# Kernel optimization log

Hardware: AMD Instinct MI355X
Metric: run time of the kernel (lower is better)

## Reference

```python
import jax, jax.numpy as jnp
import numpy as np

N_NODES = 100000
N_EDGES = 1600000
IN_F = 16
C1, C2 = 32, 64
HID = 128
N_CLASSES = 10
NUM_LAYERS = 3


def setup_inputs() -> dict:
    key = jax.random.key(0)
    ks = jax.random.split(key, 20)
    s = 0.1
    inp = {
        "x": jax.random.normal(ks[0], (N_NODES, IN_F), dtype=jnp.float32),
        "edge_index": jax.random.randint(ks[1], (2, N_EDGES), 0, N_NODES, dtype=jnp.int64),
        "edge_attr": jax.random.uniform(ks[2], (N_EDGES, 1), dtype=jnp.float32),
        # conv1 (out=32): per-step weight [L, 32, 32], GRUCell params
        "W1": jax.random.normal(ks[3], (NUM_LAYERS, C1, C1), dtype=jnp.float32) * s,
        "Wih1": jax.random.normal(ks[4], (3 * C1, C1), dtype=jnp.float32) * s,
        "Whh1": jax.random.normal(ks[5], (3 * C1, C1), dtype=jnp.float32) * s,
        "bih1": jnp.zeros((3 * C1,), dtype=jnp.float32),
        "bhh1": jnp.zeros((3 * C1,), dtype=jnp.float32),
        # conv2 (out=64)
        "W2": jax.random.normal(ks[6], (NUM_LAYERS, C2, C2), dtype=jnp.float32) * s,
        "Wih2": jax.random.normal(ks[7], (3 * C2, C2), dtype=jnp.float32) * s,
        "Whh2": jax.random.normal(ks[8], (3 * C2, C2), dtype=jnp.float32) * s,
        "bih2": jnp.zeros((3 * C2,), dtype=jnp.float32),
        "bhh2": jnp.zeros((3 * C2,), dtype=jnp.float32),
        # MLP head
        "fc1_w": jax.random.normal(ks[9], (HID, C2), dtype=jnp.float32) * s,
        "fc1_b": jnp.zeros((HID,), dtype=jnp.float32),
        "fc2_w": jax.random.normal(ks[10], (N_CLASSES, HID), dtype=jnp.float32) * s,
        "fc2_b": jnp.zeros((N_CLASSES,), dtype=jnp.float32),
    }
    return inp


def _gru_cell(m, h, Wih, Whh, bih, bhh):
    gi = m @ Wih.T + bih
    gh = h @ Whh.T + bhh
    ir, iz, inn = jnp.split(gi, 3, axis=1)
    hr, hz, hn = jnp.split(gh, 3, axis=1)
    r = jax.nn.sigmoid(ir + hr)
    z = jax.nn.sigmoid(iz + hz)
    n = jnp.tanh(inn + r * hn)
    return (1.0 - z) * n + z * h


def _gated_graph_conv(x, edge_index, edge_weight, W, Wih, Whh, bih, bhh):
    # PyG GatedGraphConv with aggr='max'
    n, c = x.shape
    out_ch = W.shape[-1]
    h = jnp.pad(x, ((0, 0), (0, out_ch - c))) if c < out_ch else x
    src, dst = edge_index[0], edge_index[1]
    ew = edge_weight[:, None]
    for i in range(W.shape[0]):
        m = h @ W[i]
        msg = m[src] * ew                      # [E, out_ch] gather + scale
        agg = jax.ops.segment_max(msg, dst, num_segments=n)  # scatter-max
        agg = jnp.where(jnp.isfinite(agg), agg, 0.0)         # empty segs -> 0
        h = _gru_cell(agg, h, Wih, Whh, bih, bhh)
    return h


def reference(x, edge_index, edge_attr, W1, Wih1, Whh1, bih1, bhh1,
              W2, Wih2, Whh2, bih2, bhh2, fc1_w, fc1_b, fc2_w, fc2_b):
    ew = jnp.squeeze(edge_attr)
    h = jax.nn.elu(_gated_graph_conv(x, edge_index, ew, W1, Wih1, Whh1, bih1, bhh1))
    h = jax.nn.elu(_gated_graph_conv(h, edge_index, ew, W2, Wih2, Whh2, bih2, bhh2))
    h = jax.nn.elu(h @ fc1_w.T + fc1_b)
    logits = h @ fc2_w.T + fc2_b
    return jax.nn.log_softmax(logits, axis=1)
```

## Files before the change

### kernel.cpp

```cpp
#include <hip/hip_runtime.h>
#include <math.h>

#define N_NODES 100000
#define N_EDGES 1600000
#define SCAN_BS 256

typedef __attribute__((ext_vector_type(8))) short bf8_t;
typedef __attribute__((ext_vector_type(4))) float f4_t;
typedef unsigned short us;

__device__ __forceinline__ float sigmoidf_(float x){ return 1.f/(1.f + expf(-x)); }
__device__ __forceinline__ float eluf_(float x){ return x > 0.f ? x : expm1f(x); }
__device__ __forceinline__ us f2bf(float x){
  unsigned u = __float_as_uint(x);
  unsigned r = u + 0x7FFFu + ((u>>16)&1u);
  return (us)(r>>16);
}
__device__ __forceinline__ float bf2f(us v){
  return __uint_as_float(((unsigned)v)<<16);
}

__global__ void prep_all(const float* __restrict__ Wih1, const float* __restrict__ Whh1,
                         const float* __restrict__ Wih2, const float* __restrict__ Whh2,
                         const float* __restrict__ W1,   const float* __restrict__ W2,
                         const float* __restrict__ fc1w, const float* __restrict__ fc2w,
                         const float* __restrict__ fc2b,
                         us* Wihb1, us* Whhb1, us* Wihb2, us* Whhb2,
                         us* Wtb1, us* Wtb2, us* fc1wb, us* fc2wpb, float* fc2bp){
  int i = blockIdx.x*256 + threadIdx.x;
  if (i < 3072) { Wihb1[i]=f2bf(Wih1[i]); return; } i -= 3072;
  if (i < 3072) { Whhb1[i]=f2bf(Whh1[i]); return; } i -= 3072;
  if (i < 12288){ Wihb2[i]=f2bf(Wih2[i]); return; } i -= 12288;
  if (i < 12288){ Whhb2[i]=f2bf(Whh2[i]); return; } i -= 12288;
  if (i < 3072) { int k=i%32, c=(i/32)%32, m=i/1024;
                  Wtb1[i]=f2bf(W1[m*1024 + k*32 + c]); return; } i -= 3072;
  if (i < 12288){ int k=i%64, c=(i/64)%64, m=i/4096;
                  Wtb2[i]=f2bf(W2[m*4096 + k*64 + c]); return; } i -= 12288;
  if (i < 8192) { fc1wb[i]=f2bf(fc1w[i]); return; } i -= 8192;
  if (i < 2048) { int c=i/128, k=i%128;
                  fc2wpb[i]=(c<10)?f2bf(fc2w[c*128+k]):(us)0; return; } i -= 2048;
  if (i < 16)   { fc2bp[i] = (i<10)? fc2b[i] : 0.f; }
}

__global__ void zero_counts(int* cnt, int* cur, int n){
  int i = blockIdx.x*blockDim.x + threadIdx.x;
  if (i < n){ cnt[i]=0; cur[i]=0; }
}
__global__ void count_kernel(const int* __restrict__ ei, int* __restrict__ cnt, int e){
  int i = blockIdx.x*blockDim.x + threadIdx.x;
  if (i < e) atomicAdd(&cnt[ei[N_EDGES + i]], 1);
}
__global__ void scan1_kernel(const int* __restrict__ cnt, int* __restrict__ pre,
                             int* __restrict__ bsum, int n){
  __shared__ int sh[SCAN_BS];
  int t = threadIdx.x, gi = blockIdx.x*SCAN_BS + t;
  int v = (gi < n) ? cnt[gi] : 0;
  sh[t] = v;
  __syncthreads();
  for (int off=1; off<SCAN_BS; off<<=1){
    int u = (t>=off)?sh[t-off]:0;
    __syncthreads();
    sh[t] += u;
    __syncthreads();
  }
  if (gi < n) pre[gi] = sh[t] - v;
  if (t == SCAN_BS-1) bsum[blockIdx.x] = sh[t];
}
__global__ void scan2_kernel(int* __restrict__ bsum, int nb){
  __shared__ int sh[1024];
  int t = threadIdx.x;
  int v = (t < nb) ? bsum[t] : 0;
  sh[t] = v;
  __syncthreads();
  for (int off=1; off<1024; off<<=1){
    int u = (t>=off)?sh[t-off]:0;
    __syncthreads();
    sh[t] += u;
    __syncthreads();
  }
  if (t < nb) bsum[t] = sh[t] - v;
}
__global__ void scan3_kernel(const int* __restrict__ pre, const int* __restrict__ bsum,
                             int* __restrict__ row_start, int n){
  int i = blockIdx.x*blockDim.x + threadIdx.x;
  if (i < n) row_start[i] = pre[i] + bsum[i/SCAN_BS];
  if (i == 0) row_start[n] = N_EDGES;
}
__global__ void scatter_kernel(const int* __restrict__ ei, const float* __restrict__ ea,
    const int* __restrict__ row_start, int* __restrict__ cur,
    long long* __restrict__ esrc, int e){
  int i0 = (blockIdx.x*blockDim.x + threadIdx.x)*2;
  #pragma unroll
  for (int j=0;j<2;j++){
    int i = i0 + j;
    if (i < e){
      int d = ei[N_EDGES + i];
      int p = row_start[d] + atomicAdd(&cur[d], 1);
      long long v = (long long)(unsigned)ei[i]
                  | ((long long)(unsigned)__float_as_int(ea[i]) << 32);
      __builtin_nontemporal_store(v, &esrc[p]);
    }
  }
}

__global__ void pad_x_kernel(const float* __restrict__ x, float* __restrict__ h,
                             us* __restrict__ hb, int n){
  int i = blockIdx.x*blockDim.x + threadIdx.x;
  if (i < n*32){
    int node = i >> 5, c = i & 31;
    float v = (c < 16) ? x[node*16 + c] : 0.f;
    h[i] = v;
    hb[i] = f2bf(v);
  }
}
__global__ void transition_kernel(const float* __restrict__ h1, float* __restrict__ h2,
                                  us* __restrict__ h2b, int n){
  int i = blockIdx.x*blockDim.x + threadIdx.x;
  if (i < n*64){
    int node = i >> 6, c = i & 63;
    float v = (c < 32) ? eluf_(h1[node*32 + c]) : 0.f;
    h2[i] = v;
    h2b[i] = f2bf(v);
  }
}

template<int C>
__global__ __launch_bounds__(256) void mgemm_mfma(const us* __restrict__ hb,
    const us* __restrict__ Wtb, us* __restrict__ mb, int n){
  constexpr int NT = C/16, KS = C/32;
  int l = threadIdx.x & 63, w = threadIdx.x >> 6;
  int mbase = blockIdx.x*64 + w*16;
  if (mbase >= n) return;
  int lr = l & 15, lk = (l >> 4)*8;
  f4_t acc[NT];
  #pragma unroll
  for (int t=0;t<NT;t++) acc[t] = f4_t{0.f,0.f,0.f,0.f};
  #pragma unroll
  for (int ks=0; ks<KS; ks++){
    int k0 = ks*32 + lk;
    bf8_t a = *(const bf8_t*)(hb + (size_t)(mbase+lr)*C + k0);
    #pragma unroll
    for (int t=0;t<NT;t++){
      bf8_t b = *(const bf8_t*)(Wtb + (size_t)(t*16+lr)*C + k0);
      acc[t] = __builtin_amdgcn_mfma_f32_16x16x32_bf16(a, b, acc[t], 0, 0, 0);
    }
  }
  int dr = (l>>4)*4;
  #pragma unroll
  for (int t=0;t<NT;t++){
    #pragma unroll
    for (int r=0;r<4;r++){
      int node = mbase + dr + r;
      if (node < n)
        mb[(size_t)node*C + t*16 + lr] = f2bf(acc[t][r]);
    }
  }
}

template<int C>
__global__ void agg_kernel(const us* __restrict__ mb, const int* __restrict__ row_start,
    const long long* __restrict__ esrc, us* __restrict__ aggb, int n_nodes){
  constexpr int GPN = C/8;
  int gid = blockIdx.x*blockDim.x + threadIdx.x;
  int nn = gid / GPN, g8 = gid % GPN;
  if (nn >= n_nodes) return;
  int s = row_start[nn], e = row_start[nn+1];
  float acc[8];
  #pragma unroll
  for (int j=0;j<8;j++) acc[j] = -__builtin_inff();
  const us* mbg = mb + g8*8;
  int i = s;
  for (; i+4<=e; i+=4){
    long long e0 = esrc[i], e1 = esrc[i+1], e2 = esrc[i+2], e3 = esrc[i+3];
    uint4 v0 = *(const uint4*)(mbg + (size_t)(unsigned)(e0 & 0xFFFFFFFF)*C);
    uint4 v1 = *(const uint4*)(mbg + (size_t)(unsigned)(e1 & 0xFFFFFFFF)*C);
    uint4 v2 = *(const uint4*)(mbg + (size_t)(unsigned)(e2 & 0xFFFFFFFF)*C);
    uint4 v3 = *(const uint4*)(mbg + (size_t)(unsigned)(e3 & 0xFFFFFFFF)*C);
    float w0 = __int_as_float((int)(e0>>32)), w1 = __int_as_float((int)(e1>>32));
    float w2 = __int_as_float((int)(e2>>32)), w3 = __int_as_float((int)(e3>>32));
    unsigned a0[4] = {v0.x, v0.y, v0.z, v0.w};
    unsigned a1[4] = {v1.x, v1.y, v1.z, v1.w};
    unsigned a2[4] = {v2.x, v2.y, v2.z, v2.w};
    unsigned a3[4] = {v3.x, v3.y, v3.z, v3.w};
    #pragma unroll
    for (int q=0;q<4;q++){
      float x0 = fmaxf(__uint_as_float(a0[q]<<16)*w0, __uint_as_float(a1[q]<<16)*w1);
      float x1 = fmaxf(__uint_as_float(a2[q]<<16)*w2, __uint_as_float(a3[q]<<16)*w3);
      float y0 = fmaxf(__uint_as_float(a0[q]&0xFFFF0000u)*w0, __uint_as_float(a1[q]&0xFFFF0000u)*w1);
      float y1 = fmaxf(__uint_as_float(a2[q]&0xFFFF0000u)*w2, __uint_as_float(a3[q]&0xFFFF0000u)*w3);
      acc[2*q]   = fmaxf(acc[2*q],   fmaxf(x0, x1));
      acc[2*q+1] = fmaxf(acc[2*q+1], fmaxf(y0, y1));
    }
  }
  for (; i<e; i++){
    long long e0 = esrc[i];
    uint4 v0 = *(const uint4*)(mbg + (size_t)(unsigned)(e0 & 0xFFFFFFFF)*C);
    float w0 = __int_as_float((int)(e0>>32));
    unsigned a0[4] = {v0.x, v0.y, v0.z, v0.w};
    #pragma unroll
    for (int q=0;q<4;q++){
      acc[2*q]   = fmaxf(acc[2*q],   __uint_as_float(a0[q]<<16)*w0);
      acc[2*q+1] = fmaxf(acc[2*q+1], __uint_as_float(a0[q]&0xFFFF0000u)*w0);
    }
  }
  unsigned r[8];
  #pragma unroll
  for (int j=0;j<8;j++) r[j] = (e > s) ? (unsigned)f2bf(acc[j]) : 0u;
  uint4 o;
  o.x = r[0] | (r[1]<<16); o.y = r[2] | (r[3]<<16);
  o.z = r[4] | (r[5]<<16); o.w = r[6] | (r[7]<<16);
  *(uint4*)(aggb + (size_t)nn*C + g8*8) = o;
}

template<int C, bool COMPUTE_M>
__global__ __launch_bounds__(256) void gru_mfma(
    const us* __restrict__ aggb, const us* __restrict__ hbin,
    const float* __restrict__ hfin,
    const us* __restrict__ Wihb, const us* __restrict__ Whhb,
    const float* __restrict__ bih, const float* __restrict__ bhh,
    const us* __restrict__ Wtb_next,
    float* __restrict__ hfout, us* __restrict__ hbout, us* __restrict__ mbout, int n){
  constexpr int NT = 3*C/16;
  constexpr int KS = C/32;
  constexpr int CT = C/16;
  constexpr int TST = C + 8;
  constexpr int TSZ = COMPUTE_M ? 16*TST : 1;
  __shared__ us tlds[4][TSZ];
  int l = threadIdx.x & 63, w = threadIdx.x >> 6;
  int mbase = blockIdx.x*64 + w*16;
  int lr = l & 15, lk = (l >> 4)*8;
  f4_t accI[NT], accH[NT];
  #pragma unroll
  for (int t=0;t<NT;t++){ accI[t]=f4_t{0.f,0.f,0.f,0.f}; accH[t]=f4_t{0.f,0.f,0.f,0.f}; }
  #pragma unroll
  for (int ks=0; ks<KS; ks++){
    int k0 = ks*32 + lk;
    bf8_t aI = *(const bf8_t*)(aggb + (size_t)(mbase+lr)*C + k0);
    bf8_t aH = *(const bf8_t*)(hbin + (size_t)(mbase+lr)*C + k0);
    #pragma unroll
    for (int t=0;t<NT;t++){
      bf8_t bI = *(const bf8_t*)(Wihb + (size_t)(t*16+lr)*C + k0);
      accI[t] = __builtin_amdgcn_mfma_f32_16x16x32_bf16(aI, bI, accI[t], 0, 0, 0);
      bf8_t bH = *(const bf8_t*)(Whhb + (size_t)(t*16+lr)*C + k0);
      accH[t] = __builtin_amdgcn_mfma_f32_16x16x32_bf16(aH, bH, accH[t], 0, 0, 0);
    }
  }
  int dr = (l>>4)*4;
  us* tile = tlds[w];
  #pragma unroll
  for (int ct=0; ct<CT; ct++){
    int c = ct*16 + lr;
    float bR = bih[c],     cR = bhh[c];
    float bZ = bih[c+C],   cZ = bhh[c+C];
    float bN = bih[c+2*C], cN = bhh[c+2*C];
    #pragma unroll
    for (int r=0;r<4;r++){
      int i = mbase + dr + r;
      float giR = accI[ct][r] + bR,      ghR = accH[ct][r] + cR;
      float giZ = accI[CT+ct][r] + bZ,   ghZ = accH[CT+ct][r] + cZ;
      float giN = accI[2*CT+ct][r] + bN, ghN = accH[2*CT+ct][r] + cN;
      float rr = sigmoidf_(giR + ghR);
      float z  = sigmoidf_(giZ + ghZ);
      float nn = tanhf(giN + rr*ghN);
      float h  = hfin[(size_t)i*C + c];
      float ho = (1.f - z)*nn + z*h;
      us hob = f2bf(ho);
      if constexpr (COMPUTE_M)
        tile[(dr+r)*TST + c] = hob;
      if (i < n){
        hfout[(size_t)i*C + c] = ho;
        hbout[(size_t)i*C + c] = hob;
      }
    }
  }
  if constexpr (COMPUTE_M){
    __syncthreads();
    f4_t macc[CT];
    #pragma unroll
    for (int t=0;t<CT;t++) macc[t] = f4_t{0.f,0.f,0.f,0.f};
    #pragma unroll
    for (int ks=0; ks<KS; ks++){
      int k0 = ks*32 + lk;
      bf8_t a = *(const bf8_t*)(tile + lr*TST + k0);
      #pragma unroll
      for (int t=0;t<CT;t++){
        bf8_t b = *(const bf8_t*)(Wtb_next + (size_t)(t*16+lr)*C + k0);
        macc[t] = __builtin_amdgcn_mfma_f32_16x16x32_bf16(a, b, macc[t], 0, 0, 0);
      }
    }
    #pragma unroll
    for (int t=0;t<CT;t++){
      #pragma unroll
      for (int r=0;r<4;r++){
        int node = mbase + dr + r;
        if (node < n)
          mbout[(size_t)node*C + t*16 + lr] = f2bf(macc[t][r]);
      }
    }
  }
}

__global__ __launch_bounds__(256) void head_mfma(const float* __restrict__ h2,
    const us* __restrict__ fc1wb, const float* __restrict__ fc1b,
    const us* __restrict__ fc2wpb, const float* __restrict__ fc2bp,
    float* __restrict__ out, int n){
  __shared__ __align__(16) us lds[4][16*136];
  int l = threadIdx.x & 63, w = threadIdx.x >> 6;
  int mbase = blockIdx.x*64 + w*16;
  int lr = l & 15, lk = (l >> 4)*8;
  int dr = (l>>4)*4;
  f4_t acc1[8];
  #pragma unroll
  for (int t=0;t<8;t++) acc1[t] = f4_t{0.f,0.f,0.f,0.f};
  #pragma unroll
  for (int ks=0; ks<2; ks++){
    int k0 = ks*32 + lk;
    const float* hp = h2 + (size_t)(mbase+lr)*64 + k0;
    float4 v0 = *(const float4*)hp;
    float4 v1 = *(const float4*)(hp+4);
    bf8_t a;
    a[0]=(short)f2bf(eluf_(v0.x)); a[1]=(short)f2bf(eluf_(v0.y));
    a[2]=(short)f2bf(eluf_(v0.z)); a[3]=(short)f2bf(eluf_(v0.w));
    a[4]=(short)f2bf(eluf_(v1.x)); a[5]=(short)f2bf(eluf_(v1.y));
    a[6]=(short)f2bf(eluf_(v1.z)); a[7]=(short)f2bf(eluf_(v1.w));
    #pragma unroll
    for (int t=0;t<8;t++){
      bf8_t b = *(const bf8_t*)(fc1wb + (size_t)(t*16+lr)*64 + k0);
      acc1[t] = __builtin_amdgcn_mfma_f32_16x16x32_bf16(a, b, acc1[t], 0, 0, 0);
    }
  }
  us* tile = lds[w];
  #pragma unroll
  for (int t=0;t<8;t++){
    float b1 = fc1b[t*16 + lr];
    #pragma unroll
    for (int r=0;r<4;r++)
      tile[(dr+r)*136 + t*16 + lr] = f2bf(eluf_(acc1[t][r] + b1));
  }
  __syncthreads();
  f4_t acc2 = f4_t{0.f,0.f,0.f,0.f};
  #pragma unroll
  for (int ks=0; ks<4; ks++){
    int k0 = ks*32 + lk;
    bf8_t a = *(const bf8_t*)(tile + lr*136 + k0);
    bf8_t b = *(const bf8_t*)(fc2wpb + (size_t)lr*128 + k0);
    acc2 = __builtin_amdgcn_mfma_f32_16x16x32_bf16(a, b, acc2, 0, 0, 0);
  }
  float b2 = fc2bp[lr];
  #pragma unroll
  for (int r=0;r<4;r++){
    float val = acc2[r] + b2;
    float vm = (lr < 10) ? val : -__builtin_inff();
    #pragma unroll
    for (int m=1;m<16;m<<=1) vm = fmaxf(vm, __shfl_xor(vm, m, 64));
    float ex = (lr < 10) ? expf(val - vm) : 0.f;
    #pragma unroll
    for (int m=1;m<16;m<<=1) ex += __shfl_xor(ex, m, 64);
    float lse = vm + logf(ex);
    int node = mbase + dr + r;
    if (lr < 10 && node < n) out[(size_t)node*10 + lr] = val - lse;
  }
}

extern "C" void kernel_launch(void* const* d_in, const int* in_sizes, int n_in,
                              void* d_out, int out_size, void* d_ws, size_t ws_size,
                              hipStream_t stream){
  const float* x    = (const float*)d_in[0];
  const int*   ei   = (const int*)  d_in[1];
  const float* ea   = (const float*)d_in[2];
  const float* W1   = (const float*)d_in[3];
  const float* Wih1 = (const float*)d_in[4];
  const float* Whh1 = (const float*)d_in[5];
  const float* bih1 = (const float*)d_in[6];
  const float* bhh1 = (const float*)d_in[7];
  const float* W2   = (const float*)d_in[8];
  const float* Wih2 = (const float*)d_in[9];
  const float* Whh2 = (const float*)d_in[10];
  const float* bih2 = (const float*)d_in[11];
  const float* bhh2 = (const float*)d_in[12];
  const float* fc1w = (const float*)d_in[13];
  const float* fc1b = (const float*)d_in[14];
  const float* fc2w = (const float*)d_in[15];
  const float* fc2b = (const float*)d_in[16];
  float* outp = (float*)d_out;

  char* ws = (char*)d_ws;
  size_t off = 0;
  auto alloc = [&](size_t bytes)->void*{
    void* p = ws + off;
    off += (bytes + 255) & ~size_t(255);
    return p;
  };
  float* hA   = (float*)alloc(sizeof(float)*N_NODES*32);
  float* hB   = (float*)alloc(sizeof(float)*N_NODES*64);
  us* hAb0    = (us*)alloc(sizeof(us)*N_NODES*32);
  us* hAb1    = (us*)alloc(sizeof(us)*N_NODES*32);
  us* hBb0    = (us*)alloc(sizeof(us)*N_NODES*64);
  us* hBb1    = (us*)alloc(sizeof(us)*N_NODES*64);
  us* mb      = (us*)alloc(sizeof(us)*N_NODES*64);
  us* aggb    = (us*)alloc(sizeof(us)*N_NODES*64);
  int* row_start = (int*)alloc(sizeof(int)*(N_NODES+1));
  int* cnt    = (int*)alloc(sizeof(int)*N_NODES);
  int* cur    = (int*)alloc(sizeof(int)*N_NODES);
  int* pre    = (int*)alloc(sizeof(int)*N_NODES);
  int* bsum   = (int*)alloc(sizeof(int)*1024);
  long long* esrc = (long long*)alloc(sizeof(long long)*N_EDGES);
  us* Wihb1   = (us*)alloc(sizeof(us)*96*32);
  us* Whhb1   = (us*)alloc(sizeof(us)*96*32);
  us* Wihb2   = (us*)alloc(sizeof(us)*192*64);
  us* Whhb2   = (us*)alloc(sizeof(us)*192*64);
  us* Wtb1    = (us*)alloc(sizeof(us)*3*32*32);
  us* Wtb2    = (us*)alloc(sizeof(us)*3*64*64);
  us* fc1wb   = (us*)alloc(sizeof(us)*128*64);
  us* fc2wpb  = (us*)alloc(sizeof(us)*16*128);
  float* fc2bp= (float*)alloc(sizeof(float)*16);
  (void)ws_size; (void)in_sizes; (void)n_in; (void)out_size;

  const int n = N_NODES, e = N_EDGES;
  const int nb = (n + SCAN_BS - 1)/SCAN_BS;
  const int gblk = (n + 63)/64;

  prep_all<<<(56336+255)/256,256,0,stream>>>(Wih1, Whh1, Wih2, Whh2, W1, W2,
      fc1w, fc2w, fc2b, Wihb1, Whhb1, Wihb2, Whhb2, Wtb1, Wtb2, fc1wb, fc2wpb, fc2bp);

  zero_counts<<<(n+255)/256,256,0,stream>>>(cnt, cur, n);
  count_kernel<<<(e+255)/256,256,0,stream>>>(ei, cnt, e);
  scan1_kernel<<<nb,SCAN_BS,0,stream>>>(cnt, pre, bsum, n);
  scan2_kernel<<<1,1024,0,stream>>>(bsum, nb);
  scan3_kernel<<<(n+255)/256,256,0,stream>>>(pre, bsum, row_start, n);
  scatter_kernel<<<(e/2+255)/256,256,0,stream>>>(ei, ea, row_start, cur, esrc, e);

  pad_x_kernel<<<(n*32+255)/256,256,0,stream>>>(x, hA, hAb0, n);
  {
    us* c0 = hAb0; us* c1 = hAb1;
    mgemm_mfma<32><<<gblk,256,0,stream>>>(c0, Wtb1, mb, n);
    for (int i=0;i<3;i++){
      agg_kernel<32><<<((long long)n*4+255)/256,256,0,stream>>>(mb, row_start, esrc, aggb, n);
      if (i < 2)
        gru_mfma<32,true><<<gblk,256,0,stream>>>(aggb, c0, hA, Wihb1, Whhb1, bih1, bhh1,
                                                 Wtb1 + (i+1)*32*32, hA, c1, mb, n);
      else
        gru_mfma<32,false><<<gblk,256,0,stream>>>(aggb, c0, hA, Wihb1, Whhb1, bih1, bhh1,
                                                  nullptr, hA, c1, nullptr, n);
      us* t = c0; c0 = c1; c1 = t;
    }
  }

  transition_kernel<<<(n*64+255)/256,256,0,stream>>>(hA, hB, hBb0, n);

  {
    us* c0 = hBb0; us* c1 = hBb1;
    mgemm_mfma<64><<<gblk,256,0,stream>>>(c0, Wtb2, mb, n);
    for (int i=0;i<3;i++){
      agg_kernel<64><<<((long long)n*8+255)/256,256,0,stream>>>(mb, row_start, esrc, aggb, n);
      if (i < 2)
        gru_mfma<64,true><<<gblk,256,0,stream>>>(aggb, c0, hB, Wihb2, Whhb2, bih2, bhh2,
                                                 Wtb2 + (i+1)*64*64, hB, c1, mb, n);
      else
        gru_mfma<64,false><<<gblk,256,0,stream>>>(aggb, c0, hB, Wihb2, Whhb2, bih2, bhh2,
                                                  nullptr, hB, c1, nullptr, n);
      us* t = c0; c0 = c1; c1 = t;
    }
  }

  head_mfma<<<gblk,256,0,stream>>>(hB, fc1wb, fc1b, fc2wpb, fc2bp, outp, n);
}
```

Before: 716.6 us.

## Bucket CSR edges by source range within each destination for gather locality

Counts and scatters edges into per-destination sub-bins keyed by the high bits of the source index, so each node's neighbor list is grouped by source range. Aggregation kernels read the same span via the bin offsets. This aims to improve cache locality of the random feature gathers. In exchange the CSR build scans and zeroes eight times as many bins, and the scan block size grows.

```diff
diff --git a/kernel.cpp b/kernel.cpp
--- a/kernel.cpp
+++ b/kernel.cpp
@@ -3,7 +3,10 @@
 
 #define N_NODES 100000
 #define N_EDGES 1600000
-#define SCAN_BS 256
+#define SCAN_BS 1024
+#define NBK 8
+#define BKSH 14
+#define NBINS (N_NODES*NBK)
 
 typedef __attribute__((ext_vector_type(8))) short bf8_t;
 typedef __attribute__((ext_vector_type(4))) float f4_t;
@@ -48,7 +51,10 @@
 }
 __global__ void count_kernel(const int* __restrict__ ei, int* __restrict__ cnt, int e){
   int i = blockIdx.x*blockDim.x + threadIdx.x;
-  if (i < e) atomicAdd(&cnt[ei[N_EDGES + i]], 1);
+  if (i < e){
+    int s = ei[i], d = ei[N_EDGES + i];
+    atomicAdd(&cnt[d*NBK + (s>>BKSH)], 1);
+  }
 }
 __global__ void scan1_kernel(const int* __restrict__ cnt, int* __restrict__ pre,
                              int* __restrict__ bsum, int n){
@@ -81,22 +87,23 @@
   if (t < nb) bsum[t] = sh[t] - v;
 }
 __global__ void scan3_kernel(const int* __restrict__ pre, const int* __restrict__ bsum,
-                             int* __restrict__ row_start, int n){
+                             int* __restrict__ rs2, int total){
   int i = blockIdx.x*blockDim.x + threadIdx.x;
-  if (i < n) row_start[i] = pre[i] + bsum[i/SCAN_BS];
-  if (i == 0) row_start[n] = N_EDGES;
+  if (i < total) rs2[i] = pre[i] + bsum[i/SCAN_BS];
+  if (i == 0) rs2[total] = N_EDGES;
 }
 __global__ void scatter_kernel(const int* __restrict__ ei, const float* __restrict__ ea,
-    const int* __restrict__ row_start, int* __restrict__ cur,
+    const int* __restrict__ rs2, int* __restrict__ cur,
     long long* __restrict__ esrc, int e){
   int i0 = (blockIdx.x*blockDim.x + threadIdx.x)*2;
   #pragma unroll
   for (int j=0;j<2;j++){
     int i = i0 + j;
     if (i < e){
-      int d = ei[N_EDGES + i];
-      int p = row_start[d] + atomicAdd(&cur[d], 1);
-      long long v = (long long)(unsigned)ei[i]
+      int s = ei[i], d = ei[N_EDGES + i];
+      int bin = d*NBK + (s>>BKSH);
+      int p = rs2[bin] + atomicAdd(&cur[bin], 1);
+      long long v = (long long)(unsigned)s
                   | ((long long)(unsigned)__float_as_int(ea[i]) << 32);
       __builtin_nontemporal_store(v, &esrc[p]);
     }
@@ -158,13 +165,13 @@
 }
 
 template<int C>
-__global__ void agg_kernel(const us* __restrict__ mb, const int* __restrict__ row_start,
+__global__ void agg_kernel(const us* __restrict__ mb, const int* __restrict__ rs2,
     const long long* __restrict__ esrc, us* __restrict__ aggb, int n_nodes){
   constexpr int GPN = C/8;
   int gid = blockIdx.x*blockDim.x + threadIdx.x;
   int nn = gid / GPN, g8 = gid % GPN;
   if (nn >= n_nodes) return;
-  int s = row_start[nn], e = row_start[nn+1];
+  int s = rs2[nn*NBK], e = rs2[nn*NBK + NBK];
   float acc[8];
   #pragma unroll
   for (int j=0;j<8;j++) acc[j] = -__builtin_inff();
@@ -399,10 +406,10 @@
   us* hBb1    = (us*)alloc(sizeof(us)*N_NODES*64);
   us* mb      = (us*)alloc(sizeof(us)*N_NODES*64);
   us* aggb    = (us*)alloc(sizeof(us)*N_NODES*64);
-  int* row_start = (int*)alloc(sizeof(int)*(N_NODES+1));
-  int* cnt    = (int*)alloc(sizeof(int)*N_NODES);
-  int* cur    = (int*)alloc(sizeof(int)*N_NODES);
-  int* pre    = (int*)alloc(sizeof(int)*N_NODES);
+  int* rs2    = (int*)alloc(sizeof(int)*(NBINS+1));
+  int* cnt    = (int*)alloc(sizeof(int)*NBINS);
+  int* cur    = (int*)alloc(sizeof(int)*NBINS);
+  int* pre    = (int*)alloc(sizeof(int)*NBINS);
   int* bsum   = (int*)alloc(sizeof(int)*1024);
   long long* esrc = (long long*)alloc(sizeof(long long)*N_EDGES);
   us* Wihb1   = (us*)alloc(sizeof(us)*96*32);
@@ -417,25 +424,25 @@
   (void)ws_size; (void)in_sizes; (void)n_in; (void)out_size;
 
   const int n = N_NODES, e = N_EDGES;
-  const int nb = (n + SCAN_BS - 1)/SCAN_BS;
+  const int nbk = (NBINS + SCAN_BS - 1)/SCAN_BS;
   const int gblk = (n + 63)/64;
 
   prep_all<<<(56336+255)/256,256,0,stream>>>(Wih1, Whh1, Wih2, Whh2, W1, W2,
       fc1w, fc2w, fc2b, Wihb1, Whhb1, Wihb2, Whhb2, Wtb1, Wtb2, fc1wb, fc2wpb, fc2bp);
 
-  zero_counts<<<(n+255)/256,256,0,stream>>>(cnt, cur, n);
+  zero_counts<<<(NBINS+255)/256,256,0,stream>>>(cnt, cur, NBINS);
   count_kernel<<<(e+255)/256,256,0,stream>>>(ei, cnt, e);
-  scan1_kernel<<<nb,SCAN_BS,0,stream>>>(cnt, pre, bsum, n);
-  scan2_kernel<<<1,1024,0,stream>>>(bsum, nb);
-  scan3_kernel<<<(n+255)/256,256,0,stream>>>(pre, bsum, row_start, n);
-  scatter_kernel<<<(e/2+255)/256,256,0,stream>>>(ei, ea, row_start, cur, esrc, e);
+  scan1_kernel<<<nbk,SCAN_BS,0,stream>>>(cnt, pre, bsum, NBINS);
+  scan2_kernel<<<1,1024,0,stream>>>(bsum, nbk);
+  scan3_kernel<<<(NBINS+255)/256,256,0,stream>>>(pre, bsum, rs2, NBINS);
+  scatter_kernel<<<(e/2+255)/256,256,0,stream>>>(ei, ea, rs2, cur, esrc, e);
 
   pad_x_kernel<<<(n*32+255)/256,256,0,stream>>>(x, hA, hAb0, n);
   {
     us* c0 = hAb0; us* c1 = hAb1;
     mgemm_mfma<32><<<gblk,256,0,stream>>>(c0, Wtb1, mb, n);
     for (int i=0;i<3;i++){
-      agg_kernel<32><<<((long long)n*4+255)/256,256,0,stream>>>(mb, row_start, esrc, aggb, n);
+      agg_kernel<32><<<((long long)n*4+255)/256,256,0,stream>>>(mb, rs2, esrc, aggb, n);
       if (i < 2)
         gru_mfma<32,true><<<gblk,256,0,stream>>>(aggb, c0, hA, Wihb1, Whhb1, bih1, bhh1,
                                                  Wtb1 + (i+1)*32*32, hA, c1, mb, n);
@@ -452,7 +459,7 @@
     us* c0 = hBb0; us* c1 = hBb1;
     mgemm_mfma<64><<<gblk,256,0,stream>>>(c0, Wtb2, mb, n);
     for (int i=0;i<3;i++){
-      agg_kernel<64><<<((long long)n*8+255)/256,256,0,stream>>>(mb, row_start, esrc, aggb, n);
+      agg_kernel<64><<<((long long)n*8+255)/256,256,0,stream>>>(mb, rs2, esrc, aggb, n);
       if (i < 2)
         gru_mfma<64,true><<<gblk,256,0,stream>>>(aggb, c0, hB, Wihb2, Whhb2, bih2, bhh2,
                                                  Wtb2 + (i+1)*64*64, hB, c1, mb, n);
```

After: 675.0 us. 1.06x faster.
